# Optimization experiments

Measured on AMD Instinct MI355X. Metric: run time of the kernel, lower is better.

Reference implementation:

```python
import jax, jax.numpy as jnp
import numpy as np

NUM_EMBEDDINGS = 1024
EMBEDDING_DIM = 64
BETA = 0.25


def setup_inputs() -> dict:
    key = jax.random.key(0)
    k1, k2 = jax.random.split(key)
    z = jax.random.normal(k1, (64, 32, 32, EMBEDDING_DIM), dtype=jnp.float32)
    emb = jax.random.uniform(
        k2, (NUM_EMBEDDINGS, EMBEDDING_DIM), dtype=jnp.float32,
        minval=-1.0 / NUM_EMBEDDINGS, maxval=1.0 / NUM_EMBEDDINGS)
    return {"z": z, "emb": emb}


def reference(z, emb):
    zf = z.reshape(-1, EMBEDDING_DIM)                      # [N, D]
    # squared L2 distances via ||z||^2 - 2 z.e + ||e||^2  -> [N, K]
    distances = (jnp.sum(zf * zf, axis=1, keepdims=True)
                 - 2.0 * jnp.matmul(zf, emb.T)
                 + jnp.sum(emb * emb, axis=1))
    encoding_indices = jnp.argmin(distances, axis=1)       # [N]
    quantized = emb[encoding_indices].reshape(z.shape)     # [B, H, W, D]
    commitment_loss = BETA * jnp.mean((jax.lax.stop_gradient(quantized) - z) ** 2)
    codebook_loss = jnp.mean((quantized - jax.lax.stop_gradient(z)) ** 2)
    loss = commitment_loss + codebook_loss
    # straight-through estimator
    quantized = z + jax.lax.stop_gradient(quantized - z)
    return (quantized, loss)
```

## Files before the change

### kernel.cpp

```cpp
#include <hip/hip_runtime.h>
#include <stdint.h>

#define N_ROWS 65536
#define K_CODES 1024
#define D 64
#define OUT_ELEMS 4194304
#define LOSS_SCALE (1.25f / 4194304.0f)
#define ROWS_PER_BLOCK 128
#define GRID_DIST (N_ROWS / ROWS_PER_BLOCK)

typedef short short8 __attribute__((ext_vector_type(8)));
typedef float f32x4 __attribute__((ext_vector_type(4)));

__device__ __forceinline__ unsigned short f2bf(float f) {
    unsigned int u = __float_as_uint(f);
    return (unsigned short)((u + 0x7fffu + ((u >> 16) & 1u)) >> 16);
}

#define GLOAD_LDS16(g, l)                                                          \
    __builtin_amdgcn_global_load_lds((const __attribute__((address_space(1))) void*)(g), \
                                     (__attribute__((address_space(3))) void*)(l), 16, 0, 0)

#define ECH (K_CODES * D / 8)
__global__ __launch_bounds__(256) void prep_kernel(const float* __restrict__ emb,
                                                   unsigned short* __restrict__ ebm2,
                                                   float* __restrict__ e2) {
    int t = blockIdx.x * 256 + threadIdx.x;
    if (t < ECH) {
        const float4* s = (const float4*)emb;
        float4 a = s[2 * t], b = s[2 * t + 1];
        uint4 o;
        o.x = f2bf(-2.f * a.x) | ((unsigned int)f2bf(-2.f * a.y) << 16);
        o.y = f2bf(-2.f * a.z) | ((unsigned int)f2bf(-2.f * a.w) << 16);
        o.z = f2bf(-2.f * b.x) | ((unsigned int)f2bf(-2.f * b.y) << 16);
        o.w = f2bf(-2.f * b.z) | ((unsigned int)f2bf(-2.f * b.w) << 16);
        ((uint4*)ebm2)[t] = o;
    } else if (t < ECH + K_CODES) {
        int k = t - ECH;
        const float4* e4 = (const float4*)emb;
        float s = 0.f;
#pragma unroll
        for (int i = 0; i < 16; i++) {
            float4 v = e4[k * 16 + i];
            s += v.x * v.x + v.y * v.y + v.z * v.z + v.w * v.w;
        }
        e2[k] = s;
    }
}

__global__ __launch_bounds__(256, 2) void dist_fused_kernel(
        const float* __restrict__ z, const unsigned short* __restrict__ ebm2,
        const float* __restrict__ e2, const float* __restrict__ emb,
        float* __restrict__ out, float* __restrict__ partials) {
    __shared__ __align__(16) char smem[65536];
    const int tid = threadIdx.x;
    const int wave = tid >> 6, lane = tid & 63;
    const int n = lane & 15, q = lane >> 4, nb = n & 7;
    const int block_row0 = blockIdx.x * ROWS_PER_BLOCK;

    short8 b[2][2];
#pragma unroll
    for (int rs = 0; rs < 2; rs++) {
        const float* zr = z + (size_t)(block_row0 + wave * 32 + rs * 16 + n) * D + q * 8;
        float4 f0 = *(const float4*)(zr);
        float4 f1 = *(const float4*)(zr + 4);
        float4 f2 = *(const float4*)(zr + 32);
        float4 f3 = *(const float4*)(zr + 36);
        short8 lo, hi;
        lo[0] = f2bf(f0.x); lo[1] = f2bf(f0.y); lo[2] = f2bf(f0.z); lo[3] = f2bf(f0.w);
        lo[4] = f2bf(f1.x); lo[5] = f2bf(f1.y); lo[6] = f2bf(f1.z); lo[7] = f2bf(f1.w);
        hi[0] = f2bf(f2.x); hi[1] = f2bf(f2.y); hi[2] = f2bf(f2.z); hi[3] = f2bf(f2.w);
        hi[4] = f2bf(f3.x); hi[5] = f2bf(f3.y); hi[6] = f2bf(f3.z); hi[7] = f2bf(f3.w);
        b[rs][0] = lo; b[rs][1] = hi;
    }

    auto stage = [&](int c) {
        const int bufoff = (c & 1) << 15;
        const uint4* gsrc = (const uint4*)ebm2;
#pragma unroll
        for (int r = 0; r < 8; r++) {
            int S = c * 2048 + r * 256 + tid;
            int P = (S & ~7) | ((S & 7) ^ ((S >> 3) & 7));
            char* l = smem + bufoff + (r * 256 + (tid & ~63)) * 16;
            GLOAD_LDS16(gsrc + P, l);
        }
    };

    f32x4 Ea = *(const f32x4*)(e2 + q * 4);
    f32x4 Eb = *(const f32x4*)(e2 + 16 + q * 4);
    const int base0 = n * 128 + ((q ^ nb) << 4);
    const int base1 = n * 128 + (((4 | q) ^ nb) << 4);

    float bestd[2] = {INFINITY, INFINITY};
    int bestk[2] = {0, 0};

    stage(0);
    __syncthreads();
    for (int c = 0; c < 4; c++) {
        if (c < 3) stage(c + 1);
        const char* buf = smem + ((c & 1) << 15);
#pragma unroll
        for (int tl = 0; tl < 16; tl++) {
            const int t = c * 16 + tl;
            short8 a0 = *(const short8*)(buf + tl * 2048 + base0);
            short8 a1 = *(const short8*)(buf + tl * 2048 + base1);
            f32x4 E = (tl & 1) ? Eb : Ea;
            f32x4 acc0 = E, acc1 = E;
            acc0 = __builtin_amdgcn_mfma_f32_16x16x32_bf16(a0, b[0][0], acc0, 0, 0, 0);
            acc0 = __builtin_amdgcn_mfma_f32_16x16x32_bf16(a1, b[0][1], acc0, 0, 0, 0);
            acc1 = __builtin_amdgcn_mfma_f32_16x16x32_bf16(a0, b[1][0], acc1, 0, 0, 0);
            acc1 = __builtin_amdgcn_mfma_f32_16x16x32_bf16(a1, b[1][1], acc1, 0, 0, 0);
            int tp = (t + 2 > 63) ? 63 : (t + 2);
            f32x4 En = *(const f32x4*)(e2 + tp * 16 + q * 4);
            if (tl & 1) Eb = En; else Ea = En;
#pragma unroll
            for (int r = 0; r < 4; r++) {
                float d0 = acc0[r];
                if (d0 < bestd[0]) { bestd[0] = d0; bestk[0] = t * 16 + q * 4 + r; }
                float d1 = acc1[r];
                if (d1 < bestd[1]) { bestd[1] = d1; bestk[1] = t * 16 + q * 4 + r; }
            }
        }
        __syncthreads();
    }

    int* sh_idx = (int*)smem;
    float* ps = (float*)(smem + 512);
#pragma unroll
    for (int rs = 0; rs < 2; rs++) {
        unsigned int db = __float_as_uint(bestd[rs]);
        db = (db & 0x80000000u) ? ~db : (db | 0x80000000u);
        unsigned long long key = ((unsigned long long)db << 32) | (unsigned int)bestk[rs];
        unsigned long long o = __shfl_xor(key, 16, 64); key = o < key ? o : key;
        o = __shfl_xor(key, 32, 64); key = o < key ? o : key;
        if (q == 0) sh_idx[wave * 32 + rs * 16 + n] = (int)(key & 0xFFFFFFFFu);
    }
    __syncthreads();

    float ssum = 0.f;
    const float4* z4 = (const float4*)z;
    float4* o4 = (float4*)out;
#pragma unroll
    for (int it = 0; it < 8; it++) {
        int cidx = it * 256 + tid;
        int lrow = cidx >> 4, d4 = cidx & 15;
        int k = sh_idx[lrow];
        size_t gi = (size_t)block_row0 * 16 + cidx;
        float4 qv = ((const float4*)emb)[k * 16 + d4];
        float4 zv = z4[gi];
        o4[gi] = qv;
        float dx = qv.x - zv.x, dy = qv.y - zv.y, dz = qv.z - zv.z, dw = qv.w - zv.w;
        ssum += dx * dx + dy * dy + dz * dz + dw * dw;
    }
#pragma unroll
    for (int off = 32; off > 0; off >>= 1)
        ssum += __shfl_down(ssum, off, 64);
    if (lane == 0) ps[wave] = ssum;
    __syncthreads();
    if (tid == 0) partials[blockIdx.x] = ps[0] + ps[1] + ps[2] + ps[3];
}

__global__ __launch_bounds__(256) void loss_kernel(const float* __restrict__ partials,
                                                   float* __restrict__ loss) {
    float s = partials[threadIdx.x] + partials[threadIdx.x + 256];
#pragma unroll
    for (int off = 32; off > 0; off >>= 1)
        s += __shfl_down(s, off, 64);
    __shared__ float ps[4];
    int wave = threadIdx.x >> 6, lane = threadIdx.x & 63;
    if (lane == 0) ps[wave] = s;
    __syncthreads();
    if (threadIdx.x == 0) loss[0] = (ps[0] + ps[1] + ps[2] + ps[3]) * LOSS_SCALE;
}

extern "C" void kernel_launch(void* const* d_in, const int* in_sizes, int n_in,
                              void* d_out, int out_size, void* d_ws, size_t ws_size,
                              hipStream_t stream) {
    const float* z = (const float*)d_in[0];
    const float* emb = (const float*)d_in[1];
    float* out = (float*)d_out;
    float* loss = out + OUT_ELEMS;

    char* ws = (char*)d_ws;
    float* e2 = (float*)ws;
    unsigned short* ebm2 = (unsigned short*)(ws + 4096);
    float* partials = (float*)(ws + 4096 + 131072 + 8192);

    prep_kernel<<<(ECH + K_CODES + 255) / 256, 256, 0, stream>>>(emb, ebm2, e2);
    dist_fused_kernel<<<GRID_DIST, 256, 0, stream>>>(z, ebm2, e2, emb, out, partials);
    loss_kernel<<<1, 256, 0, stream>>>(partials, loss);
}
```

Before: 90.27 us.

## Reuse z registers in epilogue, atomic loss accumulation, drop loss kernel

Keeps the fp32 z rows loaded for the bf16 B-fragments in registers, so the epilogue computes the squared error and writes quantized rows directly from them instead of reloading z through an LDS index table. The final loss is accumulated with one atomicAdd per block, and the zero-init moves into the prep kernel, which removes the separate reduction launch. The first codebook stage is issued before the z loads to overlap them. In exchange register pressure rises, and the atomic float sum makes the loss non-deterministic in summation order.

```diff
diff --git a/kernel.cpp b/kernel.cpp
--- a/kernel.cpp
+++ b/kernel.cpp
@@ -24,8 +24,10 @@
 #define ECH (K_CODES * D / 8)
 __global__ __launch_bounds__(256) void prep_kernel(const float* __restrict__ emb,
                                                    unsigned short* __restrict__ ebm2,
-                                                   float* __restrict__ e2) {
+                                                   float* __restrict__ e2,
+                                                   float* __restrict__ loss) {
     int t = blockIdx.x * 256 + threadIdx.x;
+    if (t == 0) loss[0] = 0.f;
     if (t < ECH) {
         const float4* s = (const float4*)emb;
         float4 a = s[2 * t], b = s[2 * t + 1];
@@ -51,28 +53,12 @@
 __global__ __launch_bounds__(256, 2) void dist_fused_kernel(
         const float* __restrict__ z, const unsigned short* __restrict__ ebm2,
         const float* __restrict__ e2, const float* __restrict__ emb,
-        float* __restrict__ out, float* __restrict__ partials) {
+        float* __restrict__ out, float* __restrict__ loss) {
     __shared__ __align__(16) char smem[65536];
     const int tid = threadIdx.x;
     const int wave = tid >> 6, lane = tid & 63;
     const int n = lane & 15, q = lane >> 4, nb = n & 7;
     const int block_row0 = blockIdx.x * ROWS_PER_BLOCK;
-
-    short8 b[2][2];
-#pragma unroll
-    for (int rs = 0; rs < 2; rs++) {
-        const float* zr = z + (size_t)(block_row0 + wave * 32 + rs * 16 + n) * D + q * 8;
-        float4 f0 = *(const float4*)(zr);
-        float4 f1 = *(const float4*)(zr + 4);
-        float4 f2 = *(const float4*)(zr + 32);
-        float4 f3 = *(const float4*)(zr + 36);
-        short8 lo, hi;
-        lo[0] = f2bf(f0.x); lo[1] = f2bf(f0.y); lo[2] = f2bf(f0.z); lo[3] = f2bf(f0.w);
-        lo[4] = f2bf(f1.x); lo[5] = f2bf(f1.y); lo[6] = f2bf(f1.z); lo[7] = f2bf(f1.w);
-        hi[0] = f2bf(f2.x); hi[1] = f2bf(f2.y); hi[2] = f2bf(f2.z); hi[3] = f2bf(f2.w);
-        hi[4] = f2bf(f3.x); hi[5] = f2bf(f3.y); hi[6] = f2bf(f3.z); hi[7] = f2bf(f3.w);
-        b[rs][0] = lo; b[rs][1] = hi;
-    }
 
     auto stage = [&](int c) {
         const int bufoff = (c & 1) << 15;
@@ -85,6 +71,25 @@
             GLOAD_LDS16(gsrc + P, l);
         }
     };
+    stage(0);
+
+    short8 b[2][2];
+    float4 zf[2][4];
+#pragma unroll
+    for (int rs = 0; rs < 2; rs++) {
+        const float* zr = z + (size_t)(block_row0 + wave * 32 + rs * 16 + n) * D + q * 8;
+        float4 f0 = *(const float4*)(zr);
+        float4 f1 = *(const float4*)(zr + 4);
+        float4 f2 = *(const float4*)(zr + 32);
+        float4 f3 = *(const float4*)(zr + 36);
+        zf[rs][0] = f0; zf[rs][1] = f1; zf[rs][2] = f2; zf[rs][3] = f3;
+        short8 lo, hi;
+        lo[0] = f2bf(f0.x); lo[1] = f2bf(f0.y); lo[2] = f2bf(f0.z); lo[3] = f2bf(f0.w);
+        lo[4] = f2bf(f1.x); lo[5] = f2bf(f1.y); lo[6] = f2bf(f1.z); lo[7] = f2bf(f1.w);
+        hi[0] = f2bf(f2.x); hi[1] = f2bf(f2.y); hi[2] = f2bf(f2.z); hi[3] = f2bf(f2.w);
+        hi[4] = f2bf(f3.x); hi[5] = f2bf(f3.y); hi[6] = f2bf(f3.z); hi[7] = f2bf(f3.w);
+        b[rs][0] = lo; b[rs][1] = hi;
+    }
 
     f32x4 Ea = *(const f32x4*)(e2 + q * 4);
     f32x4 Eb = *(const f32x4*)(e2 + 16 + q * 4);
@@ -94,7 +99,6 @@
     float bestd[2] = {INFINITY, INFINITY};
     int bestk[2] = {0, 0};
 
-    stage(0);
     __syncthreads();
     for (int c = 0; c < 4; c++) {
         if (c < 3) stage(c + 1);
@@ -124,8 +128,8 @@
         __syncthreads();
     }
 
-    int* sh_idx = (int*)smem;
-    float* ps = (float*)(smem + 512);
+    float ssum = 0.f;
+    const float4* e4 = (const float4*)emb;
 #pragma unroll
     for (int rs = 0; rs < 2; rs++) {
         unsigned int db = __float_as_uint(bestd[rs]);
@@ -133,44 +137,34 @@
         unsigned long long key = ((unsigned long long)db << 32) | (unsigned int)bestk[rs];
         unsigned long long o = __shfl_xor(key, 16, 64); key = o < key ? o : key;
         o = __shfl_xor(key, 32, 64); key = o < key ? o : key;
-        if (q == 0) sh_idx[wave * 32 + rs * 16 + n] = (int)(key & 0xFFFFFFFFu);
-    }
-    __syncthreads();
+        int k = (int)(key & 0xFFFFFFFFu);
 
-    float ssum = 0.f;
-    const float4* z4 = (const float4*)z;
-    float4* o4 = (float4*)out;
-#pragma unroll
-    for (int it = 0; it < 8; it++) {
-        int cidx = it * 256 + tid;
-        int lrow = cidx >> 4, d4 = cidx & 15;
-        int k = sh_idx[lrow];
-        size_t gi = (size_t)block_row0 * 16 + cidx;
-        float4 qv = ((const float4*)emb)[k * 16 + d4];
-        float4 zv = z4[gi];
-        o4[gi] = qv;
-        float dx = qv.x - zv.x, dy = qv.y - zv.y, dz = qv.z - zv.z, dw = qv.w - zv.w;
+        float4 q0 = e4[k * 16 + q * 2];
+        float4 q1 = e4[k * 16 + q * 2 + 1];
+        float4 q2 = e4[k * 16 + 8 + q * 2];
+        float4 q3 = e4[k * 16 + 8 + q * 2 + 1];
+        float4* orow = (float4*)(out + (size_t)(block_row0 + wave * 32 + rs * 16 + n) * D + q * 8);
+        orow[0] = q0; orow[1] = q1; orow[8] = q2; orow[9] = q3;
+
+        float4 z0 = zf[rs][0], z1 = zf[rs][1], z2 = zf[rs][2], z3 = zf[rs][3];
+        float dx, dy, dz, dw;
+        dx = q0.x - z0.x; dy = q0.y - z0.y; dz = q0.z - z0.z; dw = q0.w - z0.w;
+        ssum += dx * dx + dy * dy + dz * dz + dw * dw;
+        dx = q1.x - z1.x; dy = q1.y - z1.y; dz = q1.z - z1.z; dw = q1.w - z1.w;
+        ssum += dx * dx + dy * dy + dz * dz + dw * dw;
+        dx = q2.x - z2.x; dy = q2.y - z2.y; dz = q2.z - z2.z; dw = q2.w - z2.w;
+        ssum += dx * dx + dy * dy + dz * dz + dw * dw;
+        dx = q3.x - z3.x; dy = q3.y - z3.y; dz = q3.z - z3.z; dw = q3.w - z3.w;
         ssum += dx * dx + dy * dy + dz * dz + dw * dw;
     }
+
 #pragma unroll
     for (int off = 32; off > 0; off >>= 1)
         ssum += __shfl_down(ssum, off, 64);
+    float* ps = (float*)smem;
     if (lane == 0) ps[wave] = ssum;
     __syncthreads();
-    if (tid == 0) partials[blockIdx.x] = ps[0] + ps[1] + ps[2] + ps[3];
-}
-
-__global__ __launch_bounds__(256) void loss_kernel(const float* __restrict__ partials,
-                                                   float* __restrict__ loss) {
-    float s = partials[threadIdx.x] + partials[threadIdx.x + 256];
-#pragma unroll
-    for (int off = 32; off > 0; off >>= 1)
-        s += __shfl_down(s, off, 64);
-    __shared__ float ps[4];
-    int wave = threadIdx.x >> 6, lane = threadIdx.x & 63;
-    if (lane == 0) ps[wave] = s;
-    __syncthreads();
-    if (threadIdx.x == 0) loss[0] = (ps[0] + ps[1] + ps[2] + ps[3]) * LOSS_SCALE;
+    if (tid == 0) atomicAdd(loss, (ps[0] + ps[1] + ps[2] + ps[3]) * LOSS_SCALE);
 }
 
 extern "C" void kernel_launch(void* const* d_in, const int* in_sizes, int n_in,
@@ -184,9 +178,7 @@
     char* ws = (char*)d_ws;
     float* e2 = (float*)ws;
     unsigned short* ebm2 = (unsigned short*)(ws + 4096);
-    float* partials = (float*)(ws + 4096 + 131072 + 8192);
 
-    prep_kernel<<<(ECH + K_CODES + 255) / 256, 256, 0, stream>>>(emb, ebm2, e2);
-    dist_fused_kernel<<<GRID_DIST, 256, 0, stream>>>(z, ebm2, e2, emb, out, partials);
-    loss_kernel<<<1, 256, 0, stream>>>(partials, loss);
+    prep_kernel<<<(ECH + K_CODES + 255) / 256, 256, 0, stream>>>(emb, ebm2, e2, loss);
+    dist_fused_kernel<<<GRID_DIST, 256, 0, stream>>>(z, ebm2, e2, emb, out, loss);
 }
```

New measurement: 94.23 us. 4.4% more time.
